# Kernel optimization log

Hardware: AMD Instinct MI355X
Metric: run time of the kernel (lower is better)

The kernel has to match this reference:

```python
import jax, jax.numpy as jnp
import numpy as np

N, E = 100000, 1000000
IN_DIM, OUT_DIM, HEADS = 64, 64, 4
C = OUT_DIM // HEADS  # per-head channels = 16
NEG_SLOPE = 0.2
SOFTMAX_EPS = 1e-16  # PyG softmax denominator epsilon
LN_EPS = 1e-5


def setup_inputs() -> dict:
    key = jax.random.key(0)
    ks = jax.random.split(key, 8)
    node_input = jax.random.normal(ks[0], (N, IN_DIM), dtype=jnp.float32)
    edge_index = jax.random.randint(ks[1], (2, E), 0, N, dtype=jnp.int64)
    # GATConv params (glorot-ish scale)
    W = jax.random.normal(ks[2], (IN_DIM, HEADS * C), dtype=jnp.float32) / np.sqrt(IN_DIM)
    att_src = jax.random.normal(ks[3], (HEADS, C), dtype=jnp.float32) / np.sqrt(C)
    att_dst = jax.random.normal(ks[4], (HEADS, C), dtype=jnp.float32) / np.sqrt(C)
    bias = jnp.zeros((HEADS * C,), dtype=jnp.float32)
    # LayerNorm params
    gamma = jnp.ones((OUT_DIM,), dtype=jnp.float32)
    beta = jnp.zeros((OUT_DIM,), dtype=jnp.float32)
    return {"node_input": node_input, "edge_index": edge_index, "W": W,
            "att_src": att_src, "att_dst": att_dst, "bias": bias,
            "gamma": gamma, "beta": beta}


def _gat_forward(x, edge_index, W, att_src, att_dst, bias, gamma, beta):
    src, dst = edge_index[0], edge_index[1]  # message flows src -> dst
    h = (x @ W).reshape(N, HEADS, C)                       # [N, H, C]
    a_src = jnp.einsum('nhc,hc->nh', h, att_src)           # [N, H]
    a_dst = jnp.einsum('nhc,hc->nh', h, att_dst)           # [N, H]
    # per-edge attention logits + leaky relu
    e = a_src[src] + a_dst[dst]                            # [E, H]
    e = jnp.where(e >= 0, e, NEG_SLOPE * e)
    # segment softmax over incoming edges of each target node
    m = jax.ops.segment_max(e, dst, num_segments=N)        # [N, H]
    m = jnp.where(jnp.isfinite(m), m, 0.0)                 # empty segments -> 0
    ex = jnp.exp(e - m[dst])                               # [E, H]
    denom = jax.ops.segment_sum(ex, dst, num_segments=N)   # [N, H]
    alpha = ex / (denom[dst] + SOFTMAX_EPS)                # [E, H]
    # weighted scatter-sum of source features
    msg = alpha[:, :, None] * h[src]                       # [E, H, C]
    out = jax.ops.segment_sum(msg, dst, num_segments=N)    # [N, H, C]
    out = out.reshape(N, HEADS * C) + bias                 # concat heads + bias
    # LayerNorm
    mu = out.mean(axis=-1, keepdims=True)
    var = out.var(axis=-1, keepdims=True)
    out = (out - mu) * jax.lax.rsqrt(var + LN_EPS) * gamma + beta
    # query gate is dead code (graph is a dict -> hasattr fails); dropout is eval identity
    return out


def reference(node_input, edge_index, W, att_src, att_dst, bias, gamma, beta):
    return _gat_forward(node_input, edge_index, W, att_src, att_dst, bias, gamma, beta)
```

## Files before the change

### kernel.cpp

```cpp
#include <hip/hip_runtime.h>
#include <hip/hip_bf16.h>
#include <math.h>

#define N_NODES 100000
#define E_EDGES 1000000
#define HEADS 4
#define DIM 64
#define NEG_SLOPE 0.2f
#define SM_EPS 1e-16f
#define LN_EPS 1e-5f
#define P1_BLOCKS 256
#define NT16 6250
#define GEMM_BLOCKS 782
#define K1_BLOCKS (P1_BLOCKS + GEMM_BLOCKS)
#define CHUNK 3907
#define EPT 8
#define BUCKET_W 512
#define NBUCK 196
#define MAXE2 8

typedef __attribute__((ext_vector_type(8))) short short8v;
typedef __attribute__((ext_vector_type(4))) float f32x4;

static __device__ __forceinline__ unsigned short bfh(float f) {
    __hip_bfloat16 b = __float2bfloat16(f);
    return *reinterpret_cast<unsigned short*>(&b);
}
static __device__ __forceinline__ float bfh2f(unsigned short u) {
    return __uint_as_float((unsigned)u << 16);
}

__global__ __launch_bounds__(512) void k_feat(
        const float* __restrict__ x, const float* __restrict__ W,
        const float* __restrict__ att_src, const float* __restrict__ att_dst,
        const int* __restrict__ ei, __hip_bfloat16* __restrict__ hb,
        float* __restrict__ asrc, float* __restrict__ adst,
        int2* __restrict__ chunkbuf, int* __restrict__ pre) {
    __shared__ __align__(16) int smem_i[8326];
    int t = threadIdx.x;

    if (blockIdx.x < P1_BLOCKS) {
        int2* out2 = (int2*)smem_i;
        int*  cnt  = smem_i + 2 * CHUNK;
        int*  scan = cnt + 256;
        int base_e = blockIdx.x * CHUNK;
        int es[EPT], ed[EPT];
#pragma unroll
        for (int k = 0; k < EPT; ++k) {
            int i = k * 512 + t;
            int e = base_e + i;
            bool v = (i < CHUNK) && (e < E_EDGES);
            es[k] = v ? ei[e] : 0;
            ed[k] = v ? ei[E_EDGES + e] : -1;
        }
        if (t < 256) cnt[t] = 0;
        __syncthreads();
#pragma unroll
        for (int k = 0; k < EPT; ++k)
            if (ed[k] >= 0) atomicAdd(&cnt[ed[k] >> 9], 1);
        __syncthreads();
        if (t < 256) scan[t] = (t < NBUCK) ? cnt[t] : 0;
        __syncthreads();
#pragma unroll
        for (int off = 1; off < 256; off <<= 1) {
            int v = (t >= off && t < 256) ? scan[t - off] : 0;
            __syncthreads();
            if (t < 256) scan[t] += v;
            __syncthreads();
        }
        if (t < 256) {
            int excl = (t == 0) ? 0 : scan[t - 1];
            if (t < NBUCK) pre[blockIdx.x * (NBUCK + 1) + t] = excl;
            if (t == 0)    pre[blockIdx.x * (NBUCK + 1) + NBUCK] = scan[NBUCK - 1];
            if (t < NBUCK) cnt[t] = excl;
        }
        __syncthreads();
#pragma unroll
        for (int k = 0; k < EPT; ++k)
            if (ed[k] >= 0) {
                int pos = atomicAdd(&cnt[ed[k] >> 9], 1);
                out2[pos] = make_int2(es[k], ed[k]);
            }
        __syncthreads();
        int ec = E_EDGES - base_e; ec = (ec > CHUNK) ? CHUNK : ec;
        for (int i = t; i < ec; i += 512)
            chunkbuf[base_e + i] = out2[i];
        return;
    }

    uint4* Wlds = (uint4*)smem_i;
    for (int e = t; e < 1024; e += 512) {
        int l = e & 63, f = e >> 6;
        int s = f & 1, kh = (f >> 1) & 1, n = f >> 2;
        int c = n * 16 + (l & 15);
        int k0 = kh * 32 + (l >> 4) * 8;
        unsigned short hw[8];
#pragma unroll
        for (int j = 0; j < 8; ++j) {
            float wv = W[(k0 + j) * 64 + c];
            unsigned short hi = bfh(wv);
            hw[j] = s ? bfh(wv - bfh2f(hi)) : hi;
        }
        uint4 pk;
        pk.x = hw[0] | ((unsigned)hw[1] << 16);
        pk.y = hw[2] | ((unsigned)hw[3] << 16);
        pk.z = hw[4] | ((unsigned)hw[5] << 16);
        pk.w = hw[6] | ((unsigned)hw[7] << 16);
        Wlds[e] = pk;
    }
    __syncthreads();

    int w = t >> 6, lane = t & 63;
    int tile = (blockIdx.x - P1_BLOCKS) * 8 + w;
    if (tile >= NT16) return;
    int base = tile * 16;
    int m = lane & 15, kg = lane >> 4;

    const float* xr = x + (size_t)(base + m) * 64 + kg * 8;
    short8v ah[2], al[2];
#pragma unroll
    for (int kh = 0; kh < 2; ++kh) {
        float4 q0 = *(const float4*)(xr + kh * 32);
        float4 q1 = *(const float4*)(xr + kh * 32 + 4);
        float qq[8] = {q0.x, q0.y, q0.z, q0.w, q1.x, q1.y, q1.z, q1.w};
#pragma unroll
        for (int j = 0; j < 8; ++j) {
            unsigned short h = bfh(qq[j]);
            ah[kh][j] = (short)h;
            al[kh][j] = (short)bfh(qq[j] - bfh2f(h));
        }
    }

    const short8v* Wfv = (const short8v*)Wlds;
    float vs_keep = 0.f, vd_keep = 0.f;
#pragma unroll
    for (int n = 0; n < 4; ++n) {
        short8v bh0 = Wfv[((n * 2 + 0) * 2 + 0) * 64 + lane];
        short8v bl0 = Wfv[((n * 2 + 0) * 2 + 1) * 64 + lane];
        short8v bh1 = Wfv[((n * 2 + 1) * 2 + 0) * 64 + lane];
        short8v bl1 = Wfv[((n * 2 + 1) * 2 + 1) * 64 + lane];
        f32x4 a4 = {0.f, 0.f, 0.f, 0.f};
        a4 = __builtin_amdgcn_mfma_f32_16x16x32_bf16(ah[0], bh0, a4, 0, 0, 0);
        a4 = __builtin_amdgcn_mfma_f32_16x16x32_bf16(al[0], bh0, a4, 0, 0, 0);
        a4 = __builtin_amdgcn_mfma_f32_16x16x32_bf16(ah[0], bl0, a4, 0, 0, 0);
        a4 = __builtin_amdgcn_mfma_f32_16x16x32_bf16(ah[1], bh1, a4, 0, 0, 0);
        a4 = __builtin_amdgcn_mfma_f32_16x16x32_bf16(al[1], bh1, a4, 0, 0, 0);
        a4 = __builtin_amdgcn_mfma_f32_16x16x32_bf16(ah[1], bl1, a4, 0, 0, 0);
        float asv = att_src[n * 16 + m];
        float adv = att_dst[n * 16 + m];
#pragma unroll
        for (int ri = 0; ri < 4; ++ri) {
            int orow = base + kg * 4 + ri;
            hb[(size_t)orow * 64 + n * 16 + m] = __float2bfloat16(a4[ri]);
            float p = a4[ri] * asv, pd = a4[ri] * adv;
#pragma unroll
            for (int off = 1; off < 16; off <<= 1) {
                p  += __shfl_xor(p,  off, 64);
                pd += __shfl_xor(pd, off, 64);
            }
            if (m == ri * 4 + n) { vs_keep = p; vd_keep = pd; }
        }
    }
    asrc[tile * 64 + kg * 16 + m] = vs_keep;
    adst[tile * 64 + kg * 16 + m] = vd_keep;
}

__global__ __launch_bounds__(1024) void k_bin2(
        const int2* __restrict__ chunkbuf, const int* __restrict__ pre,
        int* __restrict__ cursorP, int* __restrict__ srclist) {
    __shared__ int cnt2[BUCKET_W];
    __shared__ int segstart[P1_BLOCKS];
    __shared__ int segpre[P1_BLOCKS + 1];
    __shared__ int scan[P1_BLOCKS];
    int t = threadIdx.x;
    int b = blockIdx.x;
    int nbase = b * BUCKET_W;
    if (t < BUCKET_W) cnt2[t] = 0;
    int p0 = 0, p1 = 0;
    if (t < 256) {
        p0 = pre[t * (NBUCK + 1) + b];
        p1 = pre[t * (NBUCK + 1) + b + 1];
        segstart[t] = t * CHUNK + p0;
        scan[t] = p0;
    }
    __syncthreads();
#pragma unroll
    for (int off = 128; off >= 1; off >>= 1) {
        int v = (t < off) ? scan[t + off] : 0;
        __syncthreads();
        if (t < off) scan[t] += v;
        __syncthreads();
    }
    int gbase = scan[0];
    __syncthreads();
    if (t < 256) scan[t] = p1 - p0;
    __syncthreads();
#pragma unroll
    for (int off = 1; off < 256; off <<= 1) {
        int v = (t >= off && t < 256) ? scan[t - off] : 0;
        __syncthreads();
        if (t < 256) scan[t] += v;
        __syncthreads();
    }
    if (t < 256) segpre[t + 1] = scan[t];
    if (t == 0) segpre[0] = 0;
    __syncthreads();
    int total = segpre[P1_BLOCKS];
    int2 ecache[MAXE2];
#pragma unroll
    for (int ii = 0; ii < MAXE2; ++ii) {
        int i = ii * 1024 + t;
        if (i < total) {
            int lo = 0, hi = P1_BLOCKS;
#pragma unroll
            for (int it = 0; it < 8; ++it) {
                int mid = (lo + hi) >> 1;
                if (segpre[mid] <= i) lo = mid; else hi = mid;
            }
            int2 e = chunkbuf[segstart[lo] + (i - segpre[lo])];
            ecache[ii] = e;
            atomicAdd(&cnt2[e.y - nbase], 1);
        }
    }
    for (int i = MAXE2 * 1024 + t; i < total; i += 1024) {
        int lo = 0, hi = P1_BLOCKS;
#pragma unroll
        for (int it = 0; it < 8; ++it) {
            int mid = (lo + hi) >> 1;
            if (segpre[mid] <= i) lo = mid; else hi = mid;
        }
        int2 e = chunkbuf[segstart[lo] + (i - segpre[lo])];
        atomicAdd(&cnt2[e.y - nbase], 1);
    }
    __syncthreads();
    int c0 = 0, c1 = 0;
    if (t < 256) {
        c0 = cnt2[2 * t]; c1 = cnt2[2 * t + 1];
        scan[t] = c0 + c1;
    }
    __syncthreads();
#pragma unroll
    for (int off = 1; off < 256; off <<= 1) {
        int v = (t >= off && t < 256) ? scan[t - off] : 0;
        __syncthreads();
        if (t < 256) scan[t] += v;
        __syncthreads();
    }
    if (t < 256) {
        int pexcl = (t == 0) ? 0 : scan[t - 1];
        cnt2[2 * t]     = pexcl;
        cnt2[2 * t + 1] = pexcl + c0;
        int n0 = nbase + 2 * t;
        if (n0 < N_NODES)     cursorP[n0]     = ((gbase + pexcl) << 6) | c0;
        if (n0 + 1 < N_NODES) cursorP[n0 + 1] = ((gbase + pexcl + c0) << 6) | c1;
    }
    __syncthreads();
#pragma unroll
    for (int ii = 0; ii < MAXE2; ++ii) {
        int i = ii * 1024 + t;
        if (i < total) {
            int2 e = ecache[ii];
            int pos = atomicAdd(&cnt2[e.y - nbase], 1);
            srclist[gbase + pos] = e.x;
        }
    }
    for (int i = MAXE2 * 1024 + t; i < total; i += 1024) {
        int lo = 0, hi = P1_BLOCKS;
#pragma unroll
        for (int it = 0; it < 8; ++it) {
            int mid = (lo + hi) >> 1;
            if (segpre[mid] <= i) lo = mid; else hi = mid;
        }
        int2 e = chunkbuf[segstart[lo] + (i - segpre[lo])];
        int pos = atomicAdd(&cnt2[e.y - nbase], 1);
        srclist[gbase + pos] = e.x;
    }
}

__global__ __launch_bounds__(256) void k_aggr(
        const int* __restrict__ cursorP, const int* __restrict__ srclist,
        const float* __restrict__ asrc, const float* __restrict__ adst,
        const __hip_bfloat16* __restrict__ hb,
        const float* __restrict__ bias, const float* __restrict__ gamma,
        const float* __restrict__ beta, float* __restrict__ out) {
    int t = threadIdx.x;
    int lane = t & 63;
    int s = lane >> 5, qq = (lane >> 4) & 1, j = lane & 15;
    int hd = j >> 2;
    int node = blockIdx.x * 8 + (t >> 6) * 2 + s;
    int cw = cursorP[node];
    int dcnt = cw & 63;
    const int* sl = srclist + ((unsigned)cw >> 6);
    const ushort4* hp = (const ushort4*)hb;
    float ad = adst[node * HEADS + hd];
    float acc0 = 0.f, acc1 = 0.f, acc2 = 0.f, acc3 = 0.f, l = 0.f;

    int idx[8];
    float as[8];
    ushort4 hv[8];
#pragma unroll
    for (int k = 0; k < 8; ++k) {
        int ek = 2 * k + qq;
        idx[k] = (ek < dcnt) ? sl[ek] : 0;
    }
#pragma unroll
    for (int k = 0; k < 8; ++k) as[k] = asrc[idx[k] * HEADS + hd];
#pragma unroll
    for (int k = 0; k < 8; ++k) hv[k] = hp[idx[k] * 16 + j];
#pragma unroll
    for (int k = 0; k < 8; ++k) {
        int ek = 2 * k + qq;
        float e = as[k] + ad;
        e = (e >= 0.f) ? e : NEG_SLOPE * e;
        float p = (ek < dcnt) ? __expf(e) : 0.f;
        l += p;
        acc0 += p * __uint_as_float((unsigned)hv[k].x << 16);
        acc1 += p * __uint_as_float((unsigned)hv[k].y << 16);
        acc2 += p * __uint_as_float((unsigned)hv[k].z << 16);
        acc3 += p * __uint_as_float((unsigned)hv[k].w << 16);
    }
    int dmax = max(dcnt, __shfl_xor(dcnt, 32, 64));
    for (int i0 = 16; i0 < dmax; i0 += 8) {
        int idt[4];
        float ast[4];
        ushort4 hvt[4];
#pragma unroll
        for (int k = 0; k < 4; ++k) {
            int ek = i0 + 2 * k + qq;
            idt[k] = (ek < dcnt) ? sl[ek] : 0;
        }
#pragma unroll
        for (int k = 0; k < 4; ++k) ast[k] = asrc[idt[k] * HEADS + hd];
#pragma unroll
        for (int k = 0; k < 4; ++k) hvt[k] = hp[idt[k] * 16 + j];
#pragma unroll
        for (int k = 0; k < 4; ++k) {
            int ek = i0 + 2 * k + qq;
            float e = ast[k] + ad;
            e = (e >= 0.f) ? e : NEG_SLOPE * e;
            float p = (ek < dcnt) ? __expf(e) : 0.f;
            l += p;
            acc0 += p * __uint_as_float((unsigned)hvt[k].x << 16);
            acc1 += p * __uint_as_float((unsigned)hvt[k].y << 16);
            acc2 += p * __uint_as_float((unsigned)hvt[k].z << 16);
            acc3 += p * __uint_as_float((unsigned)hvt[k].w << 16);
        }
    }
    acc0 += __shfl_xor(acc0, 16, 64);
    acc1 += __shfl_xor(acc1, 16, 64);
    acc2 += __shfl_xor(acc2, 16, 64);
    acc3 += __shfl_xor(acc3, 16, 64);
    l    += __shfl_xor(l,    16, 64);

    float inv = 1.f / (l + SM_EPS);
    float4 b4 = ((const float4*)bias)[j];
    float v0 = acc0 * inv + b4.x;
    float v1 = acc1 * inv + b4.y;
    float v2 = acc2 * inv + b4.z;
    float v3 = acc3 * inv + b4.w;
    float s1 = (v0 + v1) + (v2 + v3);
    float s2 = (v0 * v0 + v1 * v1) + (v2 * v2 + v3 * v3);
#pragma unroll
    for (int off = 1; off < 16; off <<= 1) {
        s1 += __shfl_xor(s1, off, 64);
        s2 += __shfl_xor(s2, off, 64);
    }
    float mu = s1 * (1.f / 64.f);
    float var = s2 * (1.f / 64.f) - mu * mu;
    float r = rsqrtf(var + LN_EPS);
    if (qq == 0) {
        float4 g4 = ((const float4*)gamma)[j];
        float4 be4 = ((const float4*)beta)[j];
        float4 o;
        o.x = (v0 - mu) * r * g4.x + be4.x;
        o.y = (v1 - mu) * r * g4.y + be4.y;
        o.z = (v2 - mu) * r * g4.z + be4.z;
        o.w = (v3 - mu) * r * g4.w + be4.w;
        ((float4*)(out + (size_t)node * DIM))[j] = o;
    }
}

extern "C" void kernel_launch(void* const* d_in, const int* in_sizes, int n_in,
                              void* d_out, int out_size, void* d_ws, size_t ws_size,
                              hipStream_t stream) {
    const float* x       = (const float*)d_in[0];
    const int*   ei      = (const int*)d_in[1];
    const float* W       = (const float*)d_in[2];
    const float* att_src = (const float*)d_in[3];
    const float* att_dst = (const float*)d_in[4];
    const float* bias    = (const float*)d_in[5];
    const float* gamma   = (const float*)d_in[6];
    const float* beta    = (const float*)d_in[7];
    float* out = (float*)d_out;

    int2* chunkbuf = (int2*)d_ws;
    int*  pre      = (int*)(chunkbuf + (size_t)P1_BLOCKS * CHUNK);
    int*  cursorP  = pre + (size_t)P1_BLOCKS * (NBUCK + 1);
    int*  srclist  = cursorP + N_NODES;
    float* asrc    = (float*)(srclist + (size_t)E_EDGES);
    float* adst    = asrc + (size_t)N_NODES * HEADS;
    __hip_bfloat16* hb = (__hip_bfloat16*)(adst + (size_t)N_NODES * HEADS);

    k_feat<<<K1_BLOCKS, 512, 0, stream>>>(x, W, att_src, att_dst, ei,
                                          hb, asrc, adst, chunkbuf, pre);
    k_bin2<<<NBUCK, 1024, 0, stream>>>(chunkbuf, pre, cursorP, srclist);
    k_aggr<<<N_NODES / 8, 256, 0, stream>>>(cursorP, srclist, asrc, adst, hb,
                                            bias, gamma, beta, out);
}
```

Before: 148.2 us.

## Precompute per-edge exp attention weights during binning, store in dst-sorted buffer

Moves the per-edge attention logit, leaky-ReLU and exp computation from the aggregation kernel into the binning kernel, writing a float4 of per-head weights per edge into a new buffer in dst-sorted order. The aggregation kernel then reads contiguous weights instead of gathering asrc by source index and computing exp. This removes a dependent random gather from the critical aggregation loop. In exchange the binning kernel does an extra random gather of asrc/adst and writes 16 MB of weights that aggregation must read back.

```diff
diff --git a/kernel.cpp b/kernel.cpp
--- a/kernel.cpp
+++ b/kernel.cpp
@@ -167,7 +167,9 @@
 
 __global__ __launch_bounds__(1024) void k_bin2(
         const int2* __restrict__ chunkbuf, const int* __restrict__ pre,
-        int* __restrict__ cursorP, int* __restrict__ srclist) {
+        const float* __restrict__ asrc, const float* __restrict__ adst,
+        int* __restrict__ cursorP, int* __restrict__ srclist,
+        float4* __restrict__ pbuf) {
     __shared__ int cnt2[BUCKET_W];
     __shared__ int segstart[P1_BLOCKS];
     __shared__ int segpre[P1_BLOCKS + 1];
@@ -175,6 +177,8 @@
     int t = threadIdx.x;
     int b = blockIdx.x;
     int nbase = b * BUCKET_W;
+    const float4* asrc4 = (const float4*)asrc;
+    const float4* adst4 = (const float4*)adst;
     if (t < BUCKET_W) cnt2[t] = 0;
     int p0 = 0, p1 = 0;
     if (t < 256) {
@@ -232,6 +236,12 @@
         int2 e = chunkbuf[segstart[lo] + (i - segpre[lo])];
         atomicAdd(&cnt2[e.y - nbase], 1);
     }
+    float4 a4c[MAXE2];
+#pragma unroll
+    for (int ii = 0; ii < MAXE2; ++ii) {
+        int i = ii * 1024 + t;
+        if (i < total) a4c[ii] = asrc4[ecache[ii].x];
+    }
     __syncthreads();
     int c0 = 0, c1 = 0;
     if (t < 256) {
@@ -262,6 +272,16 @@
             int2 e = ecache[ii];
             int pos = atomicAdd(&cnt2[e.y - nbase], 1);
             srclist[gbase + pos] = e.x;
+            float4 a4 = a4c[ii];
+            float4 d4 = adst4[e.y];
+            float4 pv;
+            float e0 = a4.x + d4.x; e0 = (e0 >= 0.f) ? e0 : NEG_SLOPE * e0;
+            float e1 = a4.y + d4.y; e1 = (e1 >= 0.f) ? e1 : NEG_SLOPE * e1;
+            float e2 = a4.z + d4.z; e2 = (e2 >= 0.f) ? e2 : NEG_SLOPE * e2;
+            float e3 = a4.w + d4.w; e3 = (e3 >= 0.f) ? e3 : NEG_SLOPE * e3;
+            pv.x = __expf(e0); pv.y = __expf(e1);
+            pv.z = __expf(e2); pv.w = __expf(e3);
+            pbuf[gbase + pos] = pv;
         }
     }
     for (int i = MAXE2 * 1024 + t; i < total; i += 1024) {
@@ -274,12 +294,22 @@
         int2 e = chunkbuf[segstart[lo] + (i - segpre[lo])];
         int pos = atomicAdd(&cnt2[e.y - nbase], 1);
         srclist[gbase + pos] = e.x;
+        float4 a4 = asrc4[e.x];
+        float4 d4 = adst4[e.y];
+        float4 pv;
+        float e0 = a4.x + d4.x; e0 = (e0 >= 0.f) ? e0 : NEG_SLOPE * e0;
+        float e1 = a4.y + d4.y; e1 = (e1 >= 0.f) ? e1 : NEG_SLOPE * e1;
+        float e2 = a4.z + d4.z; e2 = (e2 >= 0.f) ? e2 : NEG_SLOPE * e2;
+        float e3 = a4.w + d4.w; e3 = (e3 >= 0.f) ? e3 : NEG_SLOPE * e3;
+        pv.x = __expf(e0); pv.y = __expf(e1);
+        pv.z = __expf(e2); pv.w = __expf(e3);
+        pbuf[gbase + pos] = pv;
     }
 }
 
 __global__ __launch_bounds__(256) void k_aggr(
         const int* __restrict__ cursorP, const int* __restrict__ srclist,
-        const float* __restrict__ asrc, const float* __restrict__ adst,
+        const float* __restrict__ pbuf,
         const __hip_bfloat16* __restrict__ hb,
         const float* __restrict__ bias, const float* __restrict__ gamma,
         const float* __restrict__ beta, float* __restrict__ out) {
@@ -290,29 +320,27 @@
     int node = blockIdx.x * 8 + (t >> 6) * 2 + s;
     int cw = cursorP[node];
     int dcnt = cw & 63;
-    const int* sl = srclist + ((unsigned)cw >> 6);
+    int pbase = (unsigned)cw >> 6;
+    const int* sl = srclist + pbase;
+    const float* pb = pbuf + (size_t)pbase * 4 + hd;
     const ushort4* hp = (const ushort4*)hb;
-    float ad = adst[node * HEADS + hd];
     float acc0 = 0.f, acc1 = 0.f, acc2 = 0.f, acc3 = 0.f, l = 0.f;
 
     int idx[8];
-    float as[8];
+    float pv[8];
     ushort4 hv[8];
 #pragma unroll
     for (int k = 0; k < 8; ++k) {
         int ek = 2 * k + qq;
         idx[k] = (ek < dcnt) ? sl[ek] : 0;
-    }
-#pragma unroll
-    for (int k = 0; k < 8; ++k) as[k] = asrc[idx[k] * HEADS + hd];
+        pv[k] = pb[ek * 4];
+    }
 #pragma unroll
     for (int k = 0; k < 8; ++k) hv[k] = hp[idx[k] * 16 + j];
 #pragma unroll
     for (int k = 0; k < 8; ++k) {
         int ek = 2 * k + qq;
-        float e = as[k] + ad;
-        e = (e >= 0.f) ? e : NEG_SLOPE * e;
-        float p = (ek < dcnt) ? __expf(e) : 0.f;
+        float p = (ek < dcnt) ? pv[k] : 0.f;
         l += p;
         acc0 += p * __uint_as_float((unsigned)hv[k].x << 16);
         acc1 += p * __uint_as_float((unsigned)hv[k].y << 16);
@@ -322,23 +350,20 @@
     int dmax = max(dcnt, __shfl_xor(dcnt, 32, 64));
     for (int i0 = 16; i0 < dmax; i0 += 8) {
         int idt[4];
-        float ast[4];
+        float pvt[4];
         ushort4 hvt[4];
 #pragma unroll
         for (int k = 0; k < 4; ++k) {
             int ek = i0 + 2 * k + qq;
             idt[k] = (ek < dcnt) ? sl[ek] : 0;
-        }
-#pragma unroll
-        for (int k = 0; k < 4; ++k) ast[k] = asrc[idt[k] * HEADS + hd];
+            pvt[k] = pb[ek * 4];
+        }
 #pragma unroll
         for (int k = 0; k < 4; ++k) hvt[k] = hp[idt[k] * 16 + j];
 #pragma unroll
         for (int k = 0; k < 4; ++k) {
             int ek = i0 + 2 * k + qq;
-            float e = ast[k] + ad;
-            e = (e >= 0.f) ? e : NEG_SLOPE * e;
-            float p = (ek < dcnt) ? __expf(e) : 0.f;
+            float p = (ek < dcnt) ? pvt[k] : 0.f;
             l += p;
             acc0 += p * __uint_as_float((unsigned)hvt[k].x << 16);
             acc1 += p * __uint_as_float((unsigned)hvt[k].y << 16);
@@ -397,13 +422,15 @@
     int*  pre      = (int*)(chunkbuf + (size_t)P1_BLOCKS * CHUNK);
     int*  cursorP  = pre + (size_t)P1_BLOCKS * (NBUCK + 1);
     int*  srclist  = cursorP + N_NODES;
-    float* asrc    = (float*)(srclist + (size_t)E_EDGES);
+    float* asrc    = (float*)(srclist + (size_t)E_EDGES + 64);
     float* adst    = asrc + (size_t)N_NODES * HEADS;
     __hip_bfloat16* hb = (__hip_bfloat16*)(adst + (size_t)N_NODES * HEADS);
+    float4* pbuf   = (float4*)(hb + (size_t)N_NODES * DIM);
 
     k_feat<<<K1_BLOCKS, 512, 0, stream>>>(x, W, att_src, att_dst, ei,
                                           hb, asrc, adst, chunkbuf, pre);
-    k_bin2<<<NBUCK, 1024, 0, stream>>>(chunkbuf, pre, cursorP, srclist);
-    k_aggr<<<N_NODES / 8, 256, 0, stream>>>(cursorP, srclist, asrc, adst, hb,
-                                            bias, gamma, beta, out);
-}
+    k_bin2<<<NBUCK, 1024, 0, stream>>>(chunkbuf, pre, asrc, adst,
+                                       cursorP, srclist, pbuf);
+    k_aggr<<<N_NODES / 8, 256, 0, stream>>>(cursorP, srclist, (const float*)pbuf,
+                                            hb, bias, gamma, beta, out);
+}
```

Result: slower. 162.0 us (+9.3%).
